# Optimization experiments

Hardware: AMD Instinct MI355X
Metric: run time of the kernel (lower is better)

Reference implementation:

```python
import jax, jax.numpy as jnp
import numpy as np

L, B, S, H, NH, F = 4, 2, 1024, 1024, 16, 4096
DH = H // NH

def setup_inputs() -> dict:
    key = jax.random.key(0)
    ks = jax.random.split(key, 16)
    std = 0.02
    return {
        'x': jax.random.normal(ks[0], (B, S, H), jnp.float32),
        'attention_mask': jnp.ones((B, S, S), jnp.float32),
        'wq': jax.random.normal(ks[1], (L, H, H), jnp.float32) * std,
        'bq': jnp.zeros((L, H), jnp.float32),
        'wk': jax.random.normal(ks[2], (L, H, H), jnp.float32) * std,
        'bk': jnp.zeros((L, H), jnp.float32),
        'wv': jax.random.normal(ks[3], (L, H, H), jnp.float32) * std,
        'bv': jnp.zeros((L, H), jnp.float32),
        'wo_attn': jax.random.normal(ks[4], (L, H, H), jnp.float32) * std,
        'bo_attn': jnp.zeros((L, H), jnp.float32),
        'alpha_attn': jax.random.uniform(ks[5], (L,), jnp.float32) * 0.1,
        'wi': jax.random.normal(ks[6], (L, H, F), jnp.float32) * std,
        'bi': jnp.zeros((L, F), jnp.float32),
        'wo_ffn': jax.random.normal(ks[7], (L, F, H), jnp.float32) * std,
        'bo_ffn': jnp.zeros((L, H), jnp.float32),
        'alpha_ffn': jax.random.uniform(ks[8], (L,), jnp.float32) * 0.1,
    }

def _heads(t):
    # [B,S,H] -> [B,NH,S,DH]
    return t.reshape(B, S, NH, DH).transpose(0, 2, 1, 3)

def reference(x, attention_mask, wq, bq, wk, bk, wv, bv, wo_attn, bo_attn,
              alpha_attn, wi, bi, wo_ffn, bo_ffn, alpha_ffn):
    # additive mask: (1 - mask) * -10000, broadcast over heads
    adder = (1.0 - attention_mask)[:, None, :, :] * -10000.0  # [B,1,S,S]
    scale = 1.0 / jnp.sqrt(jnp.asarray(DH, x.dtype))
    for l in range(L):
        q = _heads(x @ wq[l] + bq[l])
        k = _heads(x @ wk[l] + bk[l])
        v = _heads(x @ wv[l] + bv[l])
        scores = jnp.einsum('bhqd,bhkd->bhqk', q, k) * scale + adder
        probs = jax.nn.softmax(scores, axis=-1)
        ctx = jnp.einsum('bhqk,bhkd->bhqd', probs, v)
        ctx = ctx.transpose(0, 2, 1, 3).reshape(B, S, H)
        attn_out = ctx @ wo_attn[l] + bo_attn[l]
        x = x + alpha_attn[l] * attn_out  # rezero residual
        inter = jax.nn.gelu(x @ wi[l] + bi[l], approximate=True)
        ffn_out = inter @ wo_ffn[l] + bo_ffn[l]
        x = x + alpha_ffn[l] * ffn_out  # rezero residual
    return x
```

## Files before the change

kernel.cpp:

```cpp
#include <hip/hip_runtime.h>
#include <cstdint>

#define B_  2
#define S_  1024
#define H_  1024
#define NH_ 16
#define DH_ 64
#define F_  4096
#define L_  4
#define M_  (B_*S_)

typedef __bf16 bf16;
typedef __bf16 bf16x8 __attribute__((ext_vector_type(8)));
typedef __bf16 bf16x4 __attribute__((ext_vector_type(4)));
typedef __bf16 bf16x2 __attribute__((ext_vector_type(2)));
typedef float  f32x4  __attribute__((ext_vector_type(4)));

__device__ __forceinline__ void async_ld16(void* lds, const void* g) {
  auto* lp = reinterpret_cast<__attribute__((address_space(3))) unsigned int*>(
      reinterpret_cast<uintptr_t>(lds));
  const auto* gp = reinterpret_cast<const __attribute__((address_space(1))) unsigned int*>(
      reinterpret_cast<uintptr_t>(g));
  __builtin_amdgcn_global_load_lds(gp, lp, 16, 0, 0);
}

__device__ __forceinline__ float gelu_tanh(float x) {
  float u = 0.7978845608028654f * (x + 0.044715f * x * x * x);
  u = fminf(fmaxf(u, -15.f), 15.f);
  float e = __builtin_amdgcn_exp2f(u * 2.8853900817779268f);
  return 0.5f * x * (1.f + (e - 1.f) / (e + 1.f));
}

__global__ __launch_bounds__(256) void prep_all(
    const float* __restrict__ wq, const float* __restrict__ wk,
    const float* __restrict__ wv, const float* __restrict__ wo,
    const float* __restrict__ wi, const float* __restrict__ wf,
    bf16* __restrict__ WtQKV, bf16* __restrict__ WtO,
    bf16* __restrict__ WtI, bf16* __restrict__ WtF,
    const float4* __restrict__ mask, bf16x4* __restrict__ madd,
    const float4* __restrict__ x, float4* __restrict__ xf,
    bf16x4* __restrict__ xb) {
  __shared__ __align__(16) float t[128 * 128];
  const int tid = (int)threadIdx.x;
  int idx = blockIdx.x;
  if (idx >= 3072) {
    idx -= 3072;
    if (idx < 2048) {
      const int i = idx * 256 + tid;
      const float c2 = -10000.f * 1.44269504088896f;
      float4 v = mask[i];
      bf16x4 o;
      o[0] = (bf16)((1.f - v.x) * c2);
      o[1] = (bf16)((1.f - v.y) * c2);
      o[2] = (bf16)((1.f - v.z) * c2);
      o[3] = (bf16)((1.f - v.w) * c2);
      madd[i] = o;
    } else {
      const int i = (idx - 2048) * 256 + tid;
      float4 v = x[i];
      xf[i] = v;
      bf16x4 b;
      b[0] = (bf16)v.x; b[1] = (bf16)v.y; b[2] = (bf16)v.z; b[3] = (bf16)v.w;
      xb[i] = b;
    }
    return;
  }
  const size_t HH = (size_t)H_ * H_;
  const size_t HF = (size_t)H_ * F_;
  const float* src;
  bf16* dst;
  int N, K, kk0, n0;
  if (idx < 1024) {
    const int mat = idx >> 6;
    const int s = mat >> 2, l = mat & 3;
    const int tt = idx & 63;
    kk0 = (tt >> 3) * 128; n0 = (tt & 7) * 128;
    N = H_; K = H_;
    src = (s == 0 ? wq : s == 1 ? wk : s == 2 ? wv : wo) + (size_t)l * HH;
    dst = (s < 3) ? (WtQKV + (size_t)l * 3 * HH + (size_t)s * HH)
                  : (WtO + (size_t)l * HH);
  } else if (idx < 2048) {
    const int j = idx - 1024;
    const int l = j >> 8;
    const int tt = j & 255;
    kk0 = (tt >> 5) * 128; n0 = (tt & 31) * 128;
    N = F_; K = H_;
    src = wi + (size_t)l * HF;
    dst = WtI + (size_t)l * HF;
  } else {
    const int j = idx - 2048;
    const int l = j >> 8;
    const int tt = j & 255;
    kk0 = (tt >> 3) * 128; n0 = (tt & 7) * 128;
    N = H_; K = F_;
    src = wf + (size_t)l * HF;
    dst = WtF + (size_t)l * HF;
  }
  const int w = tid >> 6, li = tid & 63;
  #pragma unroll
  for (int q = 0; q < 16; ++q) {
    const int r2 = 2 * (q * 4 + w);
    async_ld16(&t[r2 * 128],
               src + (size_t)(kk0 + r2 + (li >> 5)) * N + n0 + (li & 31) * 4);
  }
  __syncthreads();
  #pragma unroll
  for (int p = 0; p < 8; ++p) {
    const int n = p * 16 + (tid >> 4);
    const int k0 = (tid & 15) * 8;
    bf16x8 pk;
    #pragma unroll
    for (int j = 0; j < 8; ++j) pk[j] = (bf16)t[(k0 + j) * 128 + n];
    *(bf16x8*)(dst + (size_t)(n0 + n) * K + kk0 + k0) = pk;
  }
}

__device__ __forceinline__ void gemm_core(
    const bf16* __restrict__ A, const bf16* __restrict__ Bt, int ld, int kLen,
    int m0, int n0, bf16* As, bf16* Bs, f32x4 (&acc)[4][4]) {
  const int tid = (int)threadIdx.x;
  const int w = tid >> 6, l = tid & 63;
  const int lr = l & 15, lg = l >> 4;
  const int wm = w >> 1, wn = w & 1;
  const int srow = l >> 2;
  const int scol = (l & 3) * 8;

  const bf16* ag = A  + (size_t)(m0 + w * 32 + srow) * ld + scol;
  const bf16* bg = Bt + (size_t)(n0 + w * 32 + srow) * ld + scol;
  const int soff = (w * 32) * 32;

  auto stage = [&](int buf, int kk) {
    bf16* ad = As + buf * 4096 + soff;
    bf16* bd = Bs + buf * 4096 + soff;
    async_ld16(ad,           ag + kk);
    async_ld16(ad + 16 * 32, ag + kk + (size_t)16 * ld);
    async_ld16(bd,           bg + kk);
    async_ld16(bd + 16 * 32, bg + kk + (size_t)16 * ld);
  };

  stage(0, 0);
  __syncthreads();
  int cur = 0;
  for (int k0 = 0; k0 < kLen; k0 += 32) {
    if (k0 + 32 < kLen) stage(cur ^ 1, k0 + 32);
    const bf16* Ab = As + cur * 4096;
    const bf16* Bb = Bs + cur * 4096;
    bf16x8 af[4], bv[4];
    #pragma unroll
    for (int i = 0; i < 4; ++i)
      af[i] = *(const bf16x8*)(Ab + (wm * 64 + i * 16 + lr) * 32 + lg * 8);
    #pragma unroll
    for (int i = 0; i < 4; ++i)
      bv[i] = *(const bf16x8*)(Bb + (wn * 64 + i * 16 + lr) * 32 + lg * 8);
    #pragma unroll
    for (int i = 0; i < 4; ++i)
      #pragma unroll
      for (int j = 0; j < 4; ++j)
        acc[i][j] = __builtin_amdgcn_mfma_f32_16x16x32_bf16(af[i], bv[j], acc[i][j], 0, 0, 0);
    __syncthreads();
    cur ^= 1;
  }
}

template <int MODE>
__global__ __launch_bounds__(256) void gemm128_kernel(
    const bf16* __restrict__ A, const bf16* __restrict__ Bt,
    const float* __restrict__ bias, bf16* __restrict__ outb,
    int N, int K, int kSlice) {
  __shared__ __align__(16) bf16 As[2 * 128 * 32];
  __shared__ __align__(16) bf16 Bs[2 * 128 * 32];
  const int m0 = blockIdx.y * 128, n0 = blockIdx.x * 128;
  const int z = blockIdx.z;
  const f32x4 z4 = {0.f, 0.f, 0.f, 0.f};
  f32x4 acc[4][4];
  #pragma unroll
  for (int i = 0; i < 4; ++i)
    #pragma unroll
    for (int j = 0; j < 4; ++j) acc[i][j] = z4;

  gemm_core(A + (size_t)z * kSlice, Bt + (size_t)z * kSlice, K, kSlice,
            m0, n0, As, Bs, acc);

  const int tid = (int)threadIdx.x;
  const int w = tid >> 6, l = tid & 63;
  const int lr = l & 15, lg = l >> 4;
  const int wm = w >> 1, wn = w & 1;
  const size_t pbase = (MODE == 3) ? (size_t)z * M_ * (size_t)N : 0;
  #pragma unroll
  for (int i = 0; i < 4; ++i) {
    const int row0 = m0 + wm * 64 + i * 16 + lg * 4;
    #pragma unroll
    for (int j = 0; j < 4; ++j) {
      const int col = n0 + wn * 64 + j * 16 + lr;
      const float bvx = (MODE == 3) ? 0.f : bias[col];
      #pragma unroll
      for (int r = 0; r < 4; ++r) {
        const size_t idx = (size_t)(row0 + r) * N + col;
        float v = acc[i][j][r] + bvx;
        if (MODE == 3) {
          outb[pbase + idx] = (bf16)v;
        } else {
          outb[idx] = (bf16)gelu_tanh(v);
        }
      }
    }
  }
}

__global__ __launch_bounds__(256) void reduce_residual(
    const bf16x4* __restrict__ part, const float* __restrict__ bias,
    const float* __restrict__ alphap, float4* __restrict__ xf,
    bf16x4* __restrict__ xb) {
  const int i = blockIdx.x * 256 + (int)threadIdx.x;
  const int nper = M_ * H_ / 4;
  float s[4] = {0.f, 0.f, 0.f, 0.f};
  #pragma unroll
  for (int zz = 0; zz < 4; ++zz) {
    const bf16x4 p = part[i + (size_t)zz * nper];
    #pragma unroll
    for (int k = 0; k < 4; ++k) s[k] += (float)p[k];
  }
  const int col = (i * 4) & (H_ - 1);
  const float4 b4 = *(const float4*)(bias + col);
  const float a = *alphap;
  float4 xv = xf[i];
  xv.x += a * (s[0] + b4.x);
  xv.y += a * (s[1] + b4.y);
  xv.z += a * (s[2] + b4.z);
  xv.w += a * (s[3] + b4.w);
  xf[i] = xv;
  bf16x4 bb;
  bb[0] = (bf16)xv.x; bb[1] = (bf16)xv.y; bb[2] = (bf16)xv.z; bb[3] = (bf16)xv.w;
  xb[i] = bb;
}

__global__ __launch_bounds__(256) void gemm_qkv64(
    const bf16* __restrict__ A, const bf16* __restrict__ Wt,
    const float* __restrict__ bq, const float* __restrict__ bk,
    const float* __restrict__ bvv,
    bf16* __restrict__ qo, bf16* __restrict__ ko, bf16* __restrict__ vt) {
  __shared__ __align__(16) bf16 As[2 * 128 * 32];
  __shared__ __align__(16) bf16 Bs[2 * 64 * 32];
  const int tid = (int)threadIdx.x;
  const int w = tid >> 6, l = tid & 63;
  const int lr = l & 15, lg = l >> 4;
  const int wm = w >> 1, wn = w & 1;
  const int srow = l >> 2, scol = (l & 3) * 8;
  const int m0 = blockIdx.y * 128, n0 = blockIdx.x * 64;

  const bf16* ag = A  + (size_t)(m0 + w * 32 + srow) * H_ + scol;
  const bf16* bg = Wt + (size_t)(n0 + w * 16 + srow) * H_ + scol;
  const int aoff = (w * 32) * 32;
  const int boff = (w * 16) * 32;

  auto stage = [&](int buf, int kk) {
    bf16* ad = As + buf * 4096 + aoff;
    bf16* bd = Bs + buf * 2048 + boff;
    async_ld16(ad,           ag + kk);
    async_ld16(ad + 16 * 32, ag + kk + (size_t)16 * H_);
    async_ld16(bd,           bg + kk);
  };

  const f32x4 z4 = {0.f, 0.f, 0.f, 0.f};
  f32x4 acc[4][2];
  #pragma unroll
  for (int i = 0; i < 4; ++i)
    #pragma unroll
    for (int j = 0; j < 2; ++j) acc[i][j] = z4;

  stage(0, 0);
  __syncthreads();
  int cur = 0;
  for (int k0 = 0; k0 < H_; k0 += 32) {
    if (k0 + 32 < H_) stage(cur ^ 1, k0 + 32);
    const bf16* Ab = As + cur * 4096;
    const bf16* Bb = Bs + cur * 2048;
    bf16x8 af[4], bv[2];
    #pragma unroll
    for (int i = 0; i < 4; ++i)
      af[i] = *(const bf16x8*)(Ab + (wm * 64 + i * 16 + lr) * 32 + lg * 8);
    #pragma unroll
    for (int j = 0; j < 2; ++j)
      bv[j] = *(const bf16x8*)(Bb + (wn * 32 + j * 16 + lr) * 32 + lg * 8);
    #pragma unroll
    for (int i = 0; i < 4; ++i)
      #pragma unroll
      for (int j = 0; j < 2; ++j)
        acc[i][j] = __builtin_amdgcn_mfma_f32_16x16x32_bf16(af[i], bv[j], acc[i][j], 0, 0, 0);
    __syncthreads();
    cur ^= 1;
  }

  if (n0 < 2048) {
    bf16* out = (n0 < 1024) ? qo : ko;
    const float* bias = (n0 < 1024) ? bq : bk;
    const int nl = n0 & 1023;
    #pragma unroll
    for (int i = 0; i < 4; ++i) {
      const int row0 = m0 + wm * 64 + i * 16 + lg * 4;
      #pragma unroll
      for (int j = 0; j < 2; ++j) {
        const int col = nl + wn * 32 + j * 16 + lr;
        const float bvx = bias[col];
        #pragma unroll
        for (int r = 0; r < 4; ++r)
          out[(size_t)(row0 + r) * H_ + col] = (bf16)(acc[i][j][r] + bvx);
      }
    }
  } else {
    const int hh = (n0 >> 6) - 32;
    #pragma unroll
    for (int i = 0; i < 4; ++i) {
      const int row0 = m0 + wm * 64 + i * 16 + lg * 4;
      const int bb = row0 >> 10, ss = row0 & (S_ - 1);
      #pragma unroll
      for (int j = 0; j < 2; ++j) {
        const int dd = wn * 32 + j * 16 + lr;
        const float bvx = bvv[hh * 64 + dd];
        bf16x4 pk;
        #pragma unroll
        for (int r = 0; r < 4; ++r) pk[r] = (bf16)(acc[i][j][r] + bvx);
        *(bf16x4*)(vt + (((size_t)(bb * NH_ + hh) * DH_ + dd) << 10) + ss) = pk;
      }
    }
  }
}

__global__ __launch_bounds__(256) void attn_kernel7(
    const bf16* __restrict__ Q, const bf16* __restrict__ Kb,
    const bf16* __restrict__ Vt, const bf16* __restrict__ madd,
    bf16* __restrict__ Ctx) {
  const int tid = (int)threadIdx.x;
  const int w = tid >> 6, l = tid & 63;
  const int lr = l & 15, lg = l >> 4;
  const int r7 = lr & 7;
  const int h = blockIdx.y, b = blockIdx.z;
  const int q0 = blockIdx.x * 64 + w * 16;

  __shared__ __align__(16) bf16 Kt[2][64 * 64];
  __shared__ __align__(16) bf16 Vs[2][64 * 64];
  __shared__ unsigned int Pu[4][16][36];

  const bf16* qp = Q + ((size_t)(b * S_ + q0 + lr)) * H_ + h * DH_;
  const bf16x8 qa0 = *(const bf16x8*)(qp + lg * 8);
  const bf16x8 qa1 = *(const bf16x8*)(qp + 32 + lg * 8);

  const f32x4 z4 = {0.f, 0.f, 0.f, 0.f};
  f32x4 acc[4];
  #pragma unroll
  for (int dt = 0; dt < 4; ++dt) acc[dt] = z4;
  float mrow = -1e30f, ssum = 0.f;

  const bf16* Kbase = Kb + ((size_t)b * S_) * H_ + h * DH_;
  const bf16* Vbase = Vt + ((size_t)(b * NH_ + h)) * DH_ * S_;
  const bf16* Mb = madd + ((size_t)(b * S_ + q0 + lr)) * S_;

  const float c1 = 0.125f * 1.44269504088896f;
  const float THR = 10.f;

  const int sub = l >> 3;
  const int cs  = ((l & 7) ^ sub) * 8;
  auto stage = [&](int buf, int kv) {
    #pragma unroll
    for (int j = 0; j < 2; ++j) {
      const int rbase = w * 16 + j * 8;
      async_ld16(&Kt[buf][rbase * 64],
                 Kbase + (size_t)(kv + rbase + sub) * H_ + cs);
      async_ld16(&Vs[buf][rbase * 64],
                 Vbase + (size_t)(rbase + sub) * S_ + kv + cs);
    }
  };

  stage(0, 0);
  bf16x4 mk[4];
  #pragma unroll
  for (int t = 0; t < 4; ++t) mk[t] = *(const bf16x4*)(Mb + t * 16 + lg * 4);
  __syncthreads();
  int cur = 0;
  #pragma unroll 1
  for (int it = 0; it < 16; ++it) {
    const int kv0 = it * 64;
    if (it < 15) stage(cur ^ 1, kv0 + 64);
    bf16x4 mkn[4];
    if (it < 15) {
      #pragma unroll
      for (int t = 0; t < 4; ++t)
        mkn[t] = *(const bf16x4*)(Mb + kv0 + 64 + t * 16 + lg * 4);
    }
    const bf16* Kc = &Kt[cur][0];
    const bf16* Vc = &Vs[cur][0];
    bf16x8 kf0[4], kf1[4];
    #pragma unroll
    for (int t = 0; t < 4; ++t) {
      kf0[t] = *(const bf16x8*)(Kc + (t * 16 + lr) * 64 + ((lg ^ r7) * 8));
      kf1[t] = *(const bf16x8*)(Kc + (t * 16 + lr) * 64 + (((4 + lg) ^ r7) * 8));
    }
    f32x4 st[4];
    __builtin_amdgcn_s_setprio(1);
    #pragma unroll
    for (int t = 0; t < 4; ++t) {
      f32x4 s = __builtin_amdgcn_mfma_f32_16x16x32_bf16(kf0[t], qa0, z4, 0, 0, 0);
      st[t] = __builtin_amdgcn_mfma_f32_16x16x32_bf16(kf1[t], qa1, s, 0, 0, 0);
    }
    __builtin_amdgcn_s_setprio(0);
    float sv[4][4];
    #pragma unroll
    for (int t = 0; t < 4; ++t)
      #pragma unroll
      for (int r = 0; r < 4; ++r)
        sv[t][r] = st[t][r] * c1 + (float)mk[t][r];
    float nm = sv[0][0];
    #pragma unroll
    for (int t = 0; t < 4; ++t)
      #pragma unroll
      for (int r = 0; r < 4; ++r) nm = fmaxf(nm, sv[t][r]);
    nm = fmaxf(nm, __shfl_xor(nm, 16));
    nm = fmaxf(nm, __shfl_xor(nm, 32));
    if (__any(nm > mrow + THR)) {
      float newm = fmaxf(mrow, nm);
      float f = __builtin_amdgcn_exp2f(mrow - newm);
      mrow = newm;
      ssum *= f;
      #pragma unroll
      for (int dt = 0; dt < 4; ++dt)
        #pragma unroll
        for (int r = 0; r < 4; ++r) acc[dt][r] *= f;
    }
    float p[4][4];
    float ps = 0.f;
    #pragma unroll
    for (int t = 0; t < 4; ++t)
      #pragma unroll
      for (int r = 0; r < 4; ++r) {
        p[t][r] = __builtin_amdgcn_exp2f(sv[t][r] - mrow);
        ps += p[t][r];
      }
    ps += __shfl_xor(ps, 16);
    ps += __shfl_xor(ps, 32);
    ssum += ps;
    #pragma unroll
    for (int t = 0; t < 4; ++t)
      #pragma unroll
      for (int hh = 0; hh < 2; ++hh) {
        union { bf16x2 v; unsigned int u; } pk;
        pk.v[0] = (bf16)p[t][2 * hh];
        pk.v[1] = (bf16)p[t][2 * hh + 1];
        Pu[w][lr][8 * t + 2 * lg + hh] = pk.u;
      }
    const bf16x8 pf0 = *(const bf16x8*)&Pu[w][lr][4 * lg];
    const bf16x8 pf1 = *(const bf16x8*)&Pu[w][lr][16 + 4 * lg];
    __builtin_amdgcn_s_setprio(1);
    #pragma unroll
    for (int dt = 0; dt < 4; ++dt) {
      bf16x8 vb0 = *(const bf16x8*)(Vc + (dt * 16 + lr) * 64 + ((lg ^ r7) * 8));
      acc[dt] = __builtin_amdgcn_mfma_f32_16x16x32_bf16(vb0, pf0, acc[dt], 0, 0, 0);
    }
    #pragma unroll
    for (int dt = 0; dt < 4; ++dt) {
      bf16x8 vb1 = *(const bf16x8*)(Vc + (dt * 16 + lr) * 64 + (((4 + lg) ^ r7) * 8));
      acc[dt] = __builtin_amdgcn_mfma_f32_16x16x32_bf16(vb1, pf1, acc[dt], 0, 0, 0);
    }
    __builtin_amdgcn_s_setprio(0);
    if (it < 15) {
      #pragma unroll
      for (int t = 0; t < 4; ++t) mk[t] = mkn[t];
    }
    __syncthreads();
    cur ^= 1;
  }
  const float inv = 1.f / ssum;
  bf16* cp = Ctx + ((size_t)(b * S_ + q0 + lr)) * H_ + h * DH_;
  #pragma unroll
  for (int dt = 0; dt < 4; ++dt) {
    bf16x4 o;
    #pragma unroll
    for (int r = 0; r < 4; ++r) o[r] = (bf16)(acc[dt][r] * inv);
    *(bf16x4*)(cp + dt * 16 + lg * 4) = o;
  }
}

extern "C" void kernel_launch(void* const* d_in, const int* in_sizes, int n_in,
                              void* d_out, int out_size, void* d_ws, size_t ws_size,
                              hipStream_t stream) {
  (void)in_sizes; (void)n_in; (void)out_size; (void)ws_size;
  const float* x    = (const float*)d_in[0];
  const float* mask = (const float*)d_in[1];
  const float* wq   = (const float*)d_in[2];
  const float* bq   = (const float*)d_in[3];
  const float* wk   = (const float*)d_in[4];
  const float* bk   = (const float*)d_in[5];
  const float* wv   = (const float*)d_in[6];
  const float* bv   = (const float*)d_in[7];
  const float* wo   = (const float*)d_in[8];
  const float* bo   = (const float*)d_in[9];
  const float* aat  = (const float*)d_in[10];
  const float* wi   = (const float*)d_in[11];
  const float* bi   = (const float*)d_in[12];
  const float* wf   = (const float*)d_in[13];
  const float* bf_  = (const float*)d_in[14];
  const float* afn  = (const float*)d_in[15];

  char* ws = (char*)d_ws;
  size_t o = 0;
  bf16* WtQKV = (bf16*)(ws + o); o += (size_t)L_ * 3 * H_ * H_ * 2;
  bf16* WtO = (bf16*)(ws + o); o += (size_t)L_ * H_ * H_ * 2;
  bf16* WtI = (bf16*)(ws + o); o += (size_t)L_ * H_ * F_ * 2;
  bf16* WtF = (bf16*)(ws + o); o += (size_t)L_ * F_ * H_ * 2;
  bf16* madd = (bf16*)(ws + o); o += (size_t)B_ * S_ * S_ * 2;
  bf16* xb  = (bf16*)(ws + o); o += (size_t)M_ * H_ * 2;
  bf16* qb  = (bf16*)(ws + o); o += (size_t)M_ * H_ * 2;
  bf16* kbf = (bf16*)(ws + o); o += (size_t)M_ * H_ * 2;
  bf16* vt  = (bf16*)(ws + o); o += (size_t)M_ * H_ * 2;
  bf16* ctx = (bf16*)(ws + o); o += (size_t)M_ * H_ * 2;
  bf16* itm = (bf16*)(ws + o); o += (size_t)M_ * F_ * 2;
  bf16* partb = (bf16*)(ws + o); o += (size_t)4 * M_ * H_ * 2;

  float* xf = (float*)d_out;

  const size_t HH = (size_t)H_ * H_;
  prep_all<<<dim3(7168), 256, 0, stream>>>(
      wq, wk, wv, wo, wi, wf, WtQKV, WtO, WtI, WtF,
      (const float4*)mask, (bf16x4*)madd, (const float4*)x, (float4*)xf,
      (bf16x4*)xb);

  for (int l = 0; l < L_; ++l) {
    gemm_qkv64<<<dim3(48, M_/128), 256, 0, stream>>>(
        xb, WtQKV + (size_t)l * 3 * HH,
        bq + l * H_, bk + l * H_, bv + l * H_, qb, kbf, vt);
    attn_kernel7<<<dim3(S_/64, NH_, B_), 256, 0, stream>>>(
        qb, kbf, vt, madd, ctx);
    gemm128_kernel<3><<<dim3(H_/128, M_/128, 4), 256, 0, stream>>>(
        ctx, WtO + (size_t)l * HH, nullptr, partb, H_, H_, H_ / 4);
    reduce_residual<<<dim3((M_ * H_ / 4) / 256), 256, 0, stream>>>(
        (const bf16x4*)partb, bo + l * H_, aat + l, (float4*)xf, (bf16x4*)xb);
    gemm128_kernel<1><<<dim3(F_/128, M_/128), 256, 0, stream>>>(
        xb, WtI + (size_t)l * H_ * F_, bi + l * F_, itm, F_, H_, H_);
    gemm128_kernel<3><<<dim3(H_/128, M_/128, 4), 256, 0, stream>>>(
        itm, WtF + (size_t)l * F_ * H_, nullptr, partb, H_, F_, F_ / 4);
    reduce_residual<<<dim3((M_ * H_ / 4) / 256), 256, 0, stream>>>(
        (const bf16x4*)partb, bf_ + l * H_, afn + l, (float4*)xf, (bf16x4*)xb);
  }
}
```

Before: 603.7 us.

## Process two 16-row query subtiles per wave in attention to reuse K/V fragments

Each wave now handles 32 query rows (two 16-row subtiles) instead of 16, so every block covers 128 queries and the grid halves. K and V fragments read from LDS are reused across both subtiles, halving LDS and global K/V traffic per query. The cost is doubled accumulator, mask and score register state, which may lower occupancy, and fewer blocks (256) to spread across the CUs.

```diff
diff --git a/kernel.cpp b/kernel.cpp
--- a/kernel.cpp
+++ b/kernel.cpp
@@ -326,7 +326,7 @@
   }
 }
 
-__global__ __launch_bounds__(256) void attn_kernel7(
+__global__ __launch_bounds__(256) void attn_kernel8(
     const bf16* __restrict__ Q, const bf16* __restrict__ Kb,
     const bf16* __restrict__ Vt, const bf16* __restrict__ madd,
     bf16* __restrict__ Ctx) {
@@ -335,25 +335,32 @@
   const int lr = l & 15, lg = l >> 4;
   const int r7 = lr & 7;
   const int h = blockIdx.y, b = blockIdx.z;
-  const int q0 = blockIdx.x * 64 + w * 16;
+  const int q0 = blockIdx.x * 128 + w * 32;
 
   __shared__ __align__(16) bf16 Kt[2][64 * 64];
   __shared__ __align__(16) bf16 Vs[2][64 * 64];
-  __shared__ unsigned int Pu[4][16][36];
-
-  const bf16* qp = Q + ((size_t)(b * S_ + q0 + lr)) * H_ + h * DH_;
-  const bf16x8 qa0 = *(const bf16x8*)(qp + lg * 8);
-  const bf16x8 qa1 = *(const bf16x8*)(qp + 32 + lg * 8);
+  __shared__ unsigned int Pu[4][2][16][36];
+
+  bf16x8 qa0[2], qa1[2];
+  #pragma unroll
+  for (int s = 0; s < 2; ++s) {
+    const bf16* qp = Q + ((size_t)(b * S_ + q0 + 16 * s + lr)) * H_ + h * DH_;
+    qa0[s] = *(const bf16x8*)(qp + lg * 8);
+    qa1[s] = *(const bf16x8*)(qp + 32 + lg * 8);
+  }
 
   const f32x4 z4 = {0.f, 0.f, 0.f, 0.f};
-  f32x4 acc[4];
-  #pragma unroll
-  for (int dt = 0; dt < 4; ++dt) acc[dt] = z4;
-  float mrow = -1e30f, ssum = 0.f;
+  f32x4 acc[2][4];
+  #pragma unroll
+  for (int s = 0; s < 2; ++s)
+    #pragma unroll
+    for (int dt = 0; dt < 4; ++dt) acc[s][dt] = z4;
+  float mrow[2] = {-1e30f, -1e30f}, ssum[2] = {0.f, 0.f};
 
   const bf16* Kbase = Kb + ((size_t)b * S_) * H_ + h * DH_;
   const bf16* Vbase = Vt + ((size_t)(b * NH_ + h)) * DH_ * S_;
-  const bf16* Mb = madd + ((size_t)(b * S_ + q0 + lr)) * S_;
+  const bf16* Mb0 = madd + ((size_t)(b * S_ + q0 + lr)) * S_;
+  const bf16* Mb1 = madd + ((size_t)(b * S_ + q0 + 16 + lr)) * S_;
 
   const float c1 = 0.125f * 1.44269504088896f;
   const float THR = 10.f;
@@ -372,20 +379,25 @@
   };
 
   stage(0, 0);
-  bf16x4 mk[4];
-  #pragma unroll
-  for (int t = 0; t < 4; ++t) mk[t] = *(const bf16x4*)(Mb + t * 16 + lg * 4);
+  bf16x4 mk[2][4];
+  #pragma unroll
+  for (int t = 0; t < 4; ++t) {
+    mk[0][t] = *(const bf16x4*)(Mb0 + t * 16 + lg * 4);
+    mk[1][t] = *(const bf16x4*)(Mb1 + t * 16 + lg * 4);
+  }
   __syncthreads();
   int cur = 0;
   #pragma unroll 1
   for (int it = 0; it < 16; ++it) {
     const int kv0 = it * 64;
     if (it < 15) stage(cur ^ 1, kv0 + 64);
-    bf16x4 mkn[4];
+    bf16x4 mkn[2][4];
     if (it < 15) {
       #pragma unroll
-      for (int t = 0; t < 4; ++t)
-        mkn[t] = *(const bf16x4*)(Mb + kv0 + 64 + t * 16 + lg * 4);
+      for (int t = 0; t < 4; ++t) {
+        mkn[0][t] = *(const bf16x4*)(Mb0 + kv0 + 64 + t * 16 + lg * 4);
+        mkn[1][t] = *(const bf16x4*)(Mb1 + kv0 + 64 + t * 16 + lg * 4);
+      }
     }
     const bf16* Kc = &Kt[cur][0];
     const bf16* Vc = &Vs[cur][0];
@@ -395,87 +407,101 @@
       kf0[t] = *(const bf16x8*)(Kc + (t * 16 + lr) * 64 + ((lg ^ r7) * 8));
       kf1[t] = *(const bf16x8*)(Kc + (t * 16 + lr) * 64 + (((4 + lg) ^ r7) * 8));
     }
-    f32x4 st[4];
+    f32x4 st[2][4];
     __builtin_amdgcn_s_setprio(1);
     #pragma unroll
-    for (int t = 0; t < 4; ++t) {
-      f32x4 s = __builtin_amdgcn_mfma_f32_16x16x32_bf16(kf0[t], qa0, z4, 0, 0, 0);
-      st[t] = __builtin_amdgcn_mfma_f32_16x16x32_bf16(kf1[t], qa1, s, 0, 0, 0);
-    }
+    for (int s = 0; s < 2; ++s)
+      #pragma unroll
+      for (int t = 0; t < 4; ++t) {
+        f32x4 tmp = __builtin_amdgcn_mfma_f32_16x16x32_bf16(kf0[t], qa0[s], z4, 0, 0, 0);
+        st[s][t] = __builtin_amdgcn_mfma_f32_16x16x32_bf16(kf1[t], qa1[s], tmp, 0, 0, 0);
+      }
     __builtin_amdgcn_s_setprio(0);
-    float sv[4][4];
-    #pragma unroll
-    for (int t = 0; t < 4; ++t)
-      #pragma unroll
-      for (int r = 0; r < 4; ++r)
-        sv[t][r] = st[t][r] * c1 + (float)mk[t][r];
-    float nm = sv[0][0];
-    #pragma unroll
-    for (int t = 0; t < 4; ++t)
-      #pragma unroll
-      for (int r = 0; r < 4; ++r) nm = fmaxf(nm, sv[t][r]);
-    nm = fmaxf(nm, __shfl_xor(nm, 16));
-    nm = fmaxf(nm, __shfl_xor(nm, 32));
-    if (__any(nm > mrow + THR)) {
-      float newm = fmaxf(mrow, nm);
-      float f = __builtin_amdgcn_exp2f(mrow - newm);
-      mrow = newm;
-      ssum *= f;
-      #pragma unroll
-      for (int dt = 0; dt < 4; ++dt)
-        #pragma unroll
-        for (int r = 0; r < 4; ++r) acc[dt][r] *= f;
-    }
-    float p[4][4];
-    float ps = 0.f;
-    #pragma unroll
-    for (int t = 0; t < 4; ++t)
-      #pragma unroll
-      for (int r = 0; r < 4; ++r) {
-        p[t][r] = __builtin_amdgcn_exp2f(sv[t][r] - mrow);
-        ps += p[t][r];
+    #pragma unroll
+    for (int s = 0; s < 2; ++s) {
+      float sv[4][4];
+      #pragma unroll
+      for (int t = 0; t < 4; ++t)
+        #pragma unroll
+        for (int r = 0; r < 4; ++r)
+          sv[t][r] = st[s][t][r] * c1 + (float)mk[s][t][r];
+      float nm = sv[0][0];
+      #pragma unroll
+      for (int t = 0; t < 4; ++t)
+        #pragma unroll
+        for (int r = 0; r < 4; ++r) nm = fmaxf(nm, sv[t][r]);
+      nm = fmaxf(nm, __shfl_xor(nm, 16));
+      nm = fmaxf(nm, __shfl_xor(nm, 32));
+      if (__any(nm > mrow[s] + THR)) {
+        float newm = fmaxf(mrow[s], nm);
+        float f = __builtin_amdgcn_exp2f(mrow[s] - newm);
+        mrow[s] = newm;
+        ssum[s] *= f;
+        #pragma unroll
+        for (int dt = 0; dt < 4; ++dt)
+          #pragma unroll
+          for (int r = 0; r < 4; ++r) acc[s][dt][r] *= f;
       }
-    ps += __shfl_xor(ps, 16);
-    ps += __shfl_xor(ps, 32);
-    ssum += ps;
-    #pragma unroll
-    for (int t = 0; t < 4; ++t)
-      #pragma unroll
-      for (int hh = 0; hh < 2; ++hh) {
-        union { bf16x2 v; unsigned int u; } pk;
-        pk.v[0] = (bf16)p[t][2 * hh];
-        pk.v[1] = (bf16)p[t][2 * hh + 1];
-        Pu[w][lr][8 * t + 2 * lg + hh] = pk.u;
-      }
-    const bf16x8 pf0 = *(const bf16x8*)&Pu[w][lr][4 * lg];
-    const bf16x8 pf1 = *(const bf16x8*)&Pu[w][lr][16 + 4 * lg];
+      float p[4][4];
+      float ps = 0.f;
+      #pragma unroll
+      for (int t = 0; t < 4; ++t)
+        #pragma unroll
+        for (int r = 0; r < 4; ++r) {
+          p[t][r] = __builtin_amdgcn_exp2f(sv[t][r] - mrow[s]);
+          ps += p[t][r];
+        }
+      ps += __shfl_xor(ps, 16);
+      ps += __shfl_xor(ps, 32);
+      ssum[s] += ps;
+      #pragma unroll
+      for (int t = 0; t < 4; ++t)
+        #pragma unroll
+        for (int hh = 0; hh < 2; ++hh) {
+          union { bf16x2 v; unsigned int u; } pk;
+          pk.v[0] = (bf16)p[t][2 * hh];
+          pk.v[1] = (bf16)p[t][2 * hh + 1];
+          Pu[w][s][lr][8 * t + 2 * lg + hh] = pk.u;
+        }
+    }
+    const bf16x8 pf0a = *(const bf16x8*)&Pu[w][0][lr][4 * lg];
+    const bf16x8 pf1a = *(const bf16x8*)&Pu[w][0][lr][16 + 4 * lg];
+    const bf16x8 pf0b = *(const bf16x8*)&Pu[w][1][lr][4 * lg];
+    const bf16x8 pf1b = *(const bf16x8*)&Pu[w][1][lr][16 + 4 * lg];
     __builtin_amdgcn_s_setprio(1);
     #pragma unroll
     for (int dt = 0; dt < 4; ++dt) {
       bf16x8 vb0 = *(const bf16x8*)(Vc + (dt * 16 + lr) * 64 + ((lg ^ r7) * 8));
-      acc[dt] = __builtin_amdgcn_mfma_f32_16x16x32_bf16(vb0, pf0, acc[dt], 0, 0, 0);
+      acc[0][dt] = __builtin_amdgcn_mfma_f32_16x16x32_bf16(vb0, pf0a, acc[0][dt], 0, 0, 0);
+      acc[1][dt] = __builtin_amdgcn_mfma_f32_16x16x32_bf16(vb0, pf0b, acc[1][dt], 0, 0, 0);
     }
     #pragma unroll
     for (int dt = 0; dt < 4; ++dt) {
       bf16x8 vb1 = *(const bf16x8*)(Vc + (dt * 16 + lr) * 64 + (((4 + lg) ^ r7) * 8));
-      acc[dt] = __builtin_amdgcn_mfma_f32_16x16x32_bf16(vb1, pf1, acc[dt], 0, 0, 0);
+      acc[0][dt] = __builtin_amdgcn_mfma_f32_16x16x32_bf16(vb1, pf1a, acc[0][dt], 0, 0, 0);
+      acc[1][dt] = __builtin_amdgcn_mfma_f32_16x16x32_bf16(vb1, pf1b, acc[1][dt], 0, 0, 0);
     }
     __builtin_amdgcn_s_setprio(0);
     if (it < 15) {
       #pragma unroll
-      for (int t = 0; t < 4; ++t) mk[t] = mkn[t];
+      for (int s = 0; s < 2; ++s)
+        #pragma unroll
+        for (int t = 0; t < 4; ++t) mk[s][t] = mkn[s][t];
     }
     __syncthreads();
     cur ^= 1;
   }
-  const float inv = 1.f / ssum;
-  bf16* cp = Ctx + ((size_t)(b * S_ + q0 + lr)) * H_ + h * DH_;
-  #pragma unroll
-  for (int dt = 0; dt < 4; ++dt) {
-    bf16x4 o;
-    #pragma unroll
-    for (int r = 0; r < 4; ++r) o[r] = (bf16)(acc[dt][r] * inv);
-    *(bf16x4*)(cp + dt * 16 + lg * 4) = o;
+  #pragma unroll
+  for (int s = 0; s < 2; ++s) {
+    const float inv = 1.f / ssum[s];
+    bf16* cp = Ctx + ((size_t)(b * S_ + q0 + 16 * s + lr)) * H_ + h * DH_;
+    #pragma unroll
+    for (int dt = 0; dt < 4; ++dt) {
+      bf16x4 o;
+      #pragma unroll
+      for (int r = 0; r < 4; ++r) o[r] = (bf16)(acc[s][dt][r] * inv);
+      *(bf16x4*)(cp + dt * 16 + lg * 4) = o;
+    }
   }
 }
 
@@ -527,7 +553,7 @@
     gemm_qkv64<<<dim3(48, M_/128), 256, 0, stream>>>(
         xb, WtQKV + (size_t)l * 3 * HH,
         bq + l * H_, bk + l * H_, bv + l * H_, qb, kbf, vt);
-    attn_kernel7<<<dim3(S_/64, NH_, B_), 256, 0, stream>>>(
+    attn_kernel8<<<dim3(S_/128, NH_, B_), 256, 0, stream>>>(
         qb, kbf, vt, madd, ctx);
     gemm128_kernel<3><<<dim3(H_/128, M_/128, 4), 256, 0, stream>>>(
         ctx, WtO + (size_t)l * HH, nullptr, partb, H_, H_, H_ / 4);
```

Result: slower. 628.4 us (+4.1%).
